# Optimization experiments

Hardware: AMD Instinct MI355X
Metric: run time of the kernel (lower is better)

Reference implementation:

```python
import jax, jax.numpy as jnp
import numpy as np
import math

D_MODEL = 1024
N_HEAD = 16
HEAD_DIM = D_MODEL // N_HEAD
D_FF = 4096
NUM_STEPS = 100.0
RESCALE = 4000.0
EPS = 1e-5


def _sin_emb(t):
    # SinusoidalPosEmb: t scaled by rescale_steps/num_steps
    half = D_MODEL // 2
    x = t.astype(jnp.float32) / NUM_STEPS * RESCALE
    freqs = jnp.exp(jnp.arange(half, dtype=jnp.float32) * (-math.log(10000.0) / (half - 1)))
    e = x[:, None] * freqs[None, :]
    return jnp.concatenate([jnp.sin(e), jnp.cos(e)], axis=-1)


def _ln(x):
    m = jnp.mean(x, axis=-1, keepdims=True)
    v = jnp.var(x, axis=-1, keepdims=True)
    return (x - m) / jnp.sqrt(v + EPS)


def _gelu2(x):
    return x * jax.nn.sigmoid(1.702 * x)


def setup_inputs() -> dict:
    key = jax.random.key(0)
    ks = jax.random.split(key, 24)
    B, S, D, F = 4, 512, D_MODEL, D_FF
    std = 0.02
    inp = {
        'src': jax.random.normal(ks[0], (B, S, D), dtype=jnp.float32),
        'src_mask': jax.random.randint(ks[1], (B, 1, S, S), 0, 2).astype(bool),
        'timestep': jax.random.randint(ks[2], (B,), 0, 100, dtype=jnp.int32),
        'attention_bias': jax.random.normal(ks[3], (B, N_HEAD, S, S), dtype=jnp.float32),
        # AdaLayerNorm linear: D -> 2D (scale, shift)
        'W_ada': jax.random.normal(ks[4], (D, 2 * D), dtype=jnp.float32) * std,
        'b_ada': jnp.zeros((2 * D,), dtype=jnp.float32),
        'Wq': jax.random.normal(ks[5], (D, D), dtype=jnp.float32) * std,
        'bq': jnp.zeros((D,), dtype=jnp.float32),
        'Wk': jax.random.normal(ks[6], (D, D), dtype=jnp.float32) * std,
        'bk': jnp.zeros((D,), dtype=jnp.float32),
        'Wv': jax.random.normal(ks[7], (D, D), dtype=jnp.float32) * std,
        'bv': jnp.zeros((D,), dtype=jnp.float32),
        'Wo': jax.random.normal(ks[8], (D, D), dtype=jnp.float32) * std,
        'bo': jnp.zeros((D,), dtype=jnp.float32),
        'W1': jax.random.normal(ks[9], (D, F), dtype=jnp.float32) * std,
        'b1': jnp.zeros((F,), dtype=jnp.float32),
        'W2': jax.random.normal(ks[10], (F, D), dtype=jnp.float32) * std,
        'b2': jnp.zeros((D,), dtype=jnp.float32),
        'g2': jnp.ones((D,), dtype=jnp.float32),
        'beta2': jnp.zeros((D,), dtype=jnp.float32),
    }
    return inp


def reference(src, src_mask, timestep, attention_bias, W_ada, b_ada,
              Wq, bq, Wk, bk, Wv, bv, Wo, bo, W1, b1, W2, b2, g2, beta2):
    B, S, D = src.shape
    # AdaLayerNorm: LN(x) * (1 + scale) + shift, scale/shift from timestep emb
    emb = jax.nn.silu(_sin_emb(timestep)) @ W_ada + b_ada  # [B, 2D]
    scale, shift = jnp.split(emb[:, None, :], 2, axis=-1)  # each [B,1,D]
    x = _ln(src) * (1.0 + scale) + shift

    # Self-attention with spatial bias + fp32 masked softmax
    q = (x @ Wq + bq).reshape(B, S, N_HEAD, HEAD_DIM).transpose(0, 2, 1, 3)
    k = (x @ Wk + bk).reshape(B, S, N_HEAD, HEAD_DIM).transpose(0, 2, 1, 3)
    v = (x @ Wv + bv).reshape(B, S, N_HEAD, HEAD_DIM).transpose(0, 2, 1, 3)
    scores = jnp.einsum('bhqd,bhkd->bhqk', q / math.sqrt(HEAD_DIM), k)
    scores = scores + attention_bias
    scores = jnp.where(src_mask, -jnp.inf, scores.astype(jnp.float32))
    probs = jax.nn.softmax(scores, axis=-1).astype(v.dtype)
    ctx = jnp.einsum('bhqk,bhkd->bhqd', probs, v)
    ctx = ctx.transpose(0, 2, 1, 3).reshape(B, S, D)
    x = x + (ctx @ Wo + bo)  # residual from AdaLN output (as in source)

    # FFN with gelu2 on LN2(x)
    h = _ln(x) * g2 + beta2
    ff = _gelu2(h @ W1 + b1) @ W2 + b2
    return x + ff
```

## Files before the change

kernel.cpp:

```cpp
#include <hip/hip_runtime.h>
#include <math.h>

typedef __bf16 bf16x8 __attribute__((ext_vector_type(8)));
typedef float  f32x4  __attribute__((ext_vector_type(4)));
typedef unsigned short u16x8 __attribute__((ext_vector_type(8)));

__device__ __forceinline__ float bf2f(unsigned short u) {
    return __uint_as_float(((unsigned int)u) << 16);
}
__device__ __forceinline__ unsigned short f2bf_n(float f) {
    return __builtin_bit_cast(unsigned short, (__bf16)f);
}
__device__ __forceinline__ void gl_lds16(const unsigned short* g, unsigned short* l) {
    __builtin_amdgcn_global_load_lds(
        (const __attribute__((address_space(1))) unsigned int*)g,
        (__attribute__((address_space(3))) unsigned int*)l, 16, 0, 0);
}

#define BATCH 4
#define SEQ 512
#define DM 1024
#define NH 16
#define DH 64
#define DFF 4096
#define MROWS (BATCH * SEQ)

__global__ __launch_bounds__(256) void fill0_kernel(float* __restrict__ out) {
    out[blockIdx.x * 256 + threadIdx.x] = 0.0f;
}

__global__ __launch_bounds__(256) void tconv_kernel(const float* __restrict__ in,
                                                    unsigned short* __restrict__ out,
                                                    int K, int N) {
    __shared__ float tile[64][33];
    const int n0 = blockIdx.x * 32, k0 = blockIdx.y * 64;
    const int t = threadIdx.x;
    const int tx = t & 31, ty = t >> 5;
    #pragma unroll
    for (int i = 0; i < 8; ++i)
        tile[ty + i * 8][tx] = in[(size_t)(k0 + ty + i * 8) * N + n0 + tx];
    __syncthreads();
    const int nr = t >> 3;
    const int ks = (t & 7) * 8;
    u16x8 v;
    #pragma unroll
    for (int j = 0; j < 8; ++j) v[j] = f2bf_n(tile[ks + j][nr]);
    *(u16x8*)&out[(size_t)(n0 + nr) * K + k0 + ks] = v;
}

__global__ __launch_bounds__(256) void tconv4_kernel(const float* __restrict__ i0,
                                                     const float* __restrict__ i1,
                                                     const float* __restrict__ i2,
                                                     const float* __restrict__ i3,
                                                     unsigned short* __restrict__ o0,
                                                     unsigned short* __restrict__ o1,
                                                     unsigned short* __restrict__ o2,
                                                     unsigned short* __restrict__ o3) {
    const int z = blockIdx.z;
    const float* in = (z == 0) ? i0 : (z == 1) ? i1 : (z == 2) ? i2 : i3;
    unsigned short* out = (z == 0) ? o0 : (z == 1) ? o1 : (z == 2) ? o2 : o3;
    __shared__ float tile[64][33];
    const int n0 = blockIdx.x * 32, k0 = blockIdx.y * 64;
    const int t = threadIdx.x;
    const int tx = t & 31, ty = t >> 5;
    #pragma unroll
    for (int i = 0; i < 8; ++i)
        tile[ty + i * 8][tx] = in[(size_t)(k0 + ty + i * 8) * 1024 + n0 + tx];
    __syncthreads();
    const int nr = t >> 3;
    const int ks = (t & 7) * 8;
    u16x8 v;
    #pragma unroll
    for (int j = 0; j < 8; ++j) v[j] = f2bf_n(tile[ks + j][nr]);
    *(u16x8*)&out[(size_t)(n0 + nr) * 1024 + k0 + ks] = v;
}

__global__ void semb_kernel(const int* __restrict__ ts, float* __restrict__ semb) {
    int b = blockIdx.x;
    float x = (float)ts[b] * 40.0f;
    for (int j = threadIdx.x; j < 1024; j += 256) {
        int idx = (j < 512) ? j : (j - 512);
        float fr = expf(-9.210340371976184f * (float)idx / 511.0f);
        float e = x * fr;
        float v = (j < 512) ? sinf(e) : cosf(e);
        semb[b * 1024 + j] = v / (1.0f + expf(-v));
    }
}

__global__ __launch_bounds__(256) void ada_part_kernel(const float* __restrict__ semb,
                                                       const float* __restrict__ W,
                                                       float* __restrict__ part) {
    const int nb = blockIdx.x, kc = blockIdx.y;
    const int t = threadIdx.x;
    __shared__ float e_s[4][64];
    e_s[t >> 6][t & 63] = semb[(t >> 6) * 1024 + kc * 64 + (t & 63)];
    __syncthreads();
    const int n = nb * 128 + (t & 127);
    const int half = t >> 7;
    float a0 = 0.f, a1 = 0.f, a2 = 0.f, a3 = 0.f;
    const int kk0 = half * 32;
    #pragma unroll 8
    for (int kk = kk0; kk < kk0 + 32; ++kk) {
        const float w = W[(size_t)(kc * 64 + kk) * 2048 + n];
        a0 += e_s[0][kk] * w; a1 += e_s[1][kk] * w;
        a2 += e_s[2][kk] * w; a3 += e_s[3][kk] * w;
    }
    const int j = kc * 2 + half;
    float* p = part + (size_t)j * 4 * 2048 + n;
    p[0] = a0; p[2048] = a1; p[2 * 2048] = a2; p[3 * 2048] = a3;
}

__global__ __launch_bounds__(256) void ada_red_kernel(const float* __restrict__ part,
                                                      const float* __restrict__ bias,
                                                      float* __restrict__ ss) {
    const int idx = blockIdx.x * 256 + threadIdx.x;
    const int b = idx >> 11, n = idx & 2047;
    float acc = bias[n];
    #pragma unroll 8
    for (int j = 0; j < 32; ++j) acc += part[((size_t)j * 4 + b) * 2048 + n];
    ss[b * 2048 + n] = acc;
}

__global__ __launch_bounds__(256) void adaln_kernel(const float* __restrict__ src,
                                                    const float* __restrict__ ss,
                                                    unsigned short* __restrict__ xb) {
    int r = blockIdx.x;
    int b = r >> 9;
    int t = threadIdx.x;
    float4 v4 = *reinterpret_cast<const float4*>(&src[(size_t)r * DM + t * 4]);
    float v[4] = {v4.x, v4.y, v4.z, v4.w};
    float s = v[0] + v[1] + v[2] + v[3];
    float q = v[0]*v[0] + v[1]*v[1] + v[2]*v[2] + v[3]*v[3];
    #pragma unroll
    for (int off = 32; off > 0; off >>= 1) { s += __shfl_down(s, off); q += __shfl_down(q, off); }
    __shared__ float red[8];
    if ((t & 63) == 0) { red[t >> 6] = s; red[4 + (t >> 6)] = q; }
    __syncthreads();
    s = red[0] + red[1] + red[2] + red[3];
    q = red[4] + red[5] + red[6] + red[7];
    float mean = s * (1.0f / DM);
    float var = q * (1.0f / DM) - mean * mean;
    float rstd = rsqrtf(var + 1e-5f);
    ushort4 o;
    o.x = f2bf_n((v[0]-mean)*rstd*(1.0f+ss[b*2048 + t*4+0]) + ss[b*2048+1024 + t*4+0]);
    o.y = f2bf_n((v[1]-mean)*rstd*(1.0f+ss[b*2048 + t*4+1]) + ss[b*2048+1024 + t*4+1]);
    o.z = f2bf_n((v[2]-mean)*rstd*(1.0f+ss[b*2048 + t*4+2]) + ss[b*2048+1024 + t*4+2]);
    o.w = f2bf_n((v[3]-mean)*rstd*(1.0f+ss[b*2048 + t*4+3]) + ss[b*2048+1024 + t*4+3]);
    *reinterpret_cast<ushort4*>(&xb[(size_t)r * DM + t * 4]) = o;
}

__global__ __launch_bounds__(256) void ln2_kernel(const unsigned short* __restrict__ x,
                                                  const float* __restrict__ g2,
                                                  const float* __restrict__ beta2,
                                                  unsigned short* __restrict__ hout) {
    int r = blockIdx.x;
    int t = threadIdx.x;
    ushort4 s4 = *reinterpret_cast<const ushort4*>(&x[(size_t)r * DM + t * 4]);
    float v[4] = {bf2f(s4.x), bf2f(s4.y), bf2f(s4.z), bf2f(s4.w)};
    float s = v[0] + v[1] + v[2] + v[3];
    float q = v[0]*v[0] + v[1]*v[1] + v[2]*v[2] + v[3]*v[3];
    #pragma unroll
    for (int off = 32; off > 0; off >>= 1) { s += __shfl_down(s, off); q += __shfl_down(q, off); }
    __shared__ float red[8];
    if ((t & 63) == 0) { red[t >> 6] = s; red[4 + (t >> 6)] = q; }
    __syncthreads();
    s = red[0] + red[1] + red[2] + red[3];
    q = red[4] + red[5] + red[6] + red[7];
    float mean = s * (1.0f / DM);
    float var = q * (1.0f / DM) - mean * mean;
    float rstd = rsqrtf(var + 1e-5f);
    ushort4 o;
    o.x = f2bf_n((v[0]-mean)*rstd*g2[t*4+0] + beta2[t*4+0]);
    o.y = f2bf_n((v[1]-mean)*rstd*g2[t*4+1] + beta2[t*4+1]);
    o.z = f2bf_n((v[2]-mean)*rstd*g2[t*4+2] + beta2[t*4+2]);
    o.w = f2bf_n((v[3]-mean)*rstd*g2[t*4+3] + beta2[t*4+3]);
    *reinterpret_cast<ushort4*>(&hout[(size_t)r * DM + t * 4]) = o;
}

__global__ __launch_bounds__(256) void merge_kernel(const unsigned short* __restrict__ P0,
                                                    const unsigned short* __restrict__ P1,
                                                    const float* __restrict__ b2,
                                                    const unsigned short* __restrict__ x2,
                                                    float* __restrict__ out) {
    const size_t i4 = ((size_t)blockIdx.x * 256 + threadIdx.x) * 4;
    const int c = (int)(i4 & 1023);
    ushort4 p0 = *(const ushort4*)&P0[i4];
    ushort4 p1 = *(const ushort4*)&P1[i4];
    ushort4 xx = *(const ushort4*)&x2[i4];
    float4 bb = *(const float4*)&b2[c];
    float4 o;
    o.x = bf2f(p0.x) + bf2f(p1.x) + bb.x + bf2f(xx.x);
    o.y = bf2f(p0.y) + bf2f(p1.y) + bb.y + bf2f(xx.y);
    o.z = bf2f(p0.z) + bf2f(p1.z) + bb.z + bf2f(xx.z);
    o.w = bf2f(p0.w) + bf2f(p1.w) + bb.w + bf2f(xx.w);
    *(float4*)&out[i4] = o;
}

template<int MODE, int TN, int SELMODE>
__global__ __launch_bounds__(256) void gemm_gl(
    const unsigned short* __restrict__ A,
    const unsigned short* __restrict__ Wta, const unsigned short* __restrict__ Wtb,
    const unsigned short* __restrict__ Wtc,
    const float* __restrict__ ba, const float* __restrict__ bbb, const float* __restrict__ bc,
    const unsigned short* __restrict__ resid,
    unsigned short* __restrict__ oa, unsigned short* __restrict__ ob,
    unsigned short* __restrict__ oc,
    float* __restrict__ outF,
    int M, int N, int K, int lda, int ldk)
{
    constexpr int CR  = 128 + TN;
    constexpr int RPW = CR / 4;
    constexpr int NI  = RPW / 8;
    constexpr int WAVE_N = (TN == 128) ? 2 : 1;
    constexpr int WAVE_M = 4 / WAVE_N;
    constexpr int AM = 128 / (WAVE_M * 16);
    constexpr int AN = TN / (WAVE_N * 16);
    constexpr int BUF = CR * 64;

    __shared__ unsigned short LDSu[2 * BUF];

    const int gx = gridDim.x, gy = gridDim.y;
    const int nwg = gx * gy * gridDim.z;
    const int wid = blockIdx.x + gx * (blockIdx.y + gy * blockIdx.z);
    const int aid = (wid & 7) * (nwg >> 3) + (wid >> 3);
    const int plane = gx * gy;
    const int sel = aid / plane;
    const int pid = aid % plane;
    const int by = pid % gy;
    const int bx = pid / gy;

    const unsigned short* Wt;
    const float* bias;
    unsigned short* outB;
    int koff;
    if (SELMODE == 0) {
        Wt = (sel == 0) ? Wta : (sel == 1) ? Wtb : Wtc;
        bias = (sel == 0) ? ba : (sel == 1) ? bbb : bc;
        outB = (sel == 0) ? oa : (sel == 1) ? ob : oc;
        koff = 0;
    } else {
        Wt = Wta; bias = ba;
        outB = (sel == 0) ? oa : ob;
        koff = sel * K;
    }

    const int t = threadIdx.x;
    const int lane = t & 63;
    const int w = t >> 6;
    const int l15 = lane & 15, l4 = lane >> 4;
    const int wm = w / WAVE_N, wn = w % WAVE_N;
    const int m0 = by * 128, n0 = bx * TN;

    f32x4 acc[AM][AN];
    #pragma unroll
    for (int i = 0; i < AM; ++i)
        #pragma unroll
        for (int j = 0; j < AN; ++j)
            #pragma unroll
            for (int r = 0; r < 4; ++r) acc[i][j][r] = 0.0f;

    const int gg = (lane & 7) ^ (lane >> 3);
    const unsigned short* gp[NI];
    unsigned short* lp[NI];
    #pragma unroll
    for (int i = 0; i < NI; ++i) {
        const int cr = w * RPW + i * 8 + (lane >> 3);
        gp[i] = (cr < 128) ? (A + (size_t)(m0 + cr) * lda + koff + gg * 8)
                           : (Wt + (size_t)(n0 + cr - 128) * ldk + koff + gg * 8);
        lp[i] = LDSu + (w * RPW + i * 8) * 64;
    }

    const int NT = K / 64;
    #pragma unroll
    for (int i = 0; i < NI; ++i) gl_lds16(gp[i], lp[i]);
    __syncthreads();

    for (int kt = 0; kt < NT; ++kt) {
        const int cur = kt & 1;
        if (kt + 1 < NT) {
            const int k0 = (kt + 1) * 64;
            const int nxo = (cur ^ 1) * BUF;
            #pragma unroll
            for (int i = 0; i < NI; ++i) gl_lds16(gp[i] + k0, lp[i] + nxo);
        }
        const unsigned short* Lb = LDSu + cur * BUF;
        #pragma unroll
        for (int kk = 0; kk < 2; ++kk) {
            const int slot = ((kk * 4 + l4) ^ (l15 & 7)) * 8;
            bf16x8 af[AM], bfr[AN];
            #pragma unroll
            for (int mt = 0; mt < AM; ++mt) {
                const int row = wm * (AM * 16) + mt * 16 + l15;
                u16x8 tmp = *(const u16x8*)(Lb + row * 64 + slot);
                af[mt] = __builtin_bit_cast(bf16x8, tmp);
            }
            #pragma unroll
            for (int nt = 0; nt < AN; ++nt) {
                const int row = 128 + wn * (AN * 16) + nt * 16 + l15;
                u16x8 tmp = *(const u16x8*)(Lb + row * 64 + slot);
                bfr[nt] = __builtin_bit_cast(bf16x8, tmp);
            }
            #pragma unroll
            for (int mt = 0; mt < AM; ++mt)
                #pragma unroll
                for (int nt = 0; nt < AN; ++nt)
                    acc[mt][nt] = __builtin_amdgcn_mfma_f32_16x16x32_bf16(
                        af[mt], bfr[nt], acc[mt][nt], 0, 0, 0);
        }
        if (kt + 1 < NT) __syncthreads();
    }

    #pragma unroll
    for (int mt = 0; mt < AM; ++mt) {
        const int mbase = m0 + wm * (AM * 16) + mt * 16 + l4 * 4;
        #pragma unroll
        for (int nt = 0; nt < AN; ++nt) {
            const int n = n0 + wn * (AN * 16) + nt * 16 + l15;
            const float bs = (MODE == 5) ? 0.0f : bias[n];
            #pragma unroll
            for (int r = 0; r < 4; ++r) {
                const int m = mbase + r;
                float v = acc[mt][nt][r] + bs;
                if (MODE == 2) v = v / (1.0f + expf(-1.702f * v));
                if (MODE == 1 || MODE == 3) v += bf2f(resid[(size_t)m * N + n]);
                if (MODE == 3) outF[(size_t)m * N + n] = v;
                else           outB[(size_t)m * N + n] = f2bf_n(v);
            }
        }
    }
}

#define QB2 32
#define AKT 64
#define KROW 72
#define VROW 72
#define PROW 72
#define SBPIT 72

__global__ __launch_bounds__(128) void attn_mfma(const unsigned short* __restrict__ qbuf,
                                                 const unsigned short* __restrict__ kbuf,
                                                 const unsigned short* __restrict__ vbuf,
                                                 const float* __restrict__ attb,
                                                 const int* __restrict__ mask,
                                                 unsigned short* __restrict__ ctx) {
    __shared__ unsigned short Ks[AKT * KROW];
    __shared__ unsigned short Vt[DH * VROW];
    __shared__ unsigned short Pb[2 * 16 * PROW];
    __shared__ unsigned short Sb[QB2 * SBPIT];
    const int t = threadIdx.x;
    const int lane = t & 63;
    const int w = t >> 6;
    const int l15 = lane & 15, l4 = lane >> 4;
    const int q0 = blockIdx.x * QB2;
    const int h = blockIdx.y;
    const int b = blockIdx.z;

    bf16x8 qf[2];
    {
        const unsigned short* qrow = qbuf + ((size_t)(b * SEQ + q0 + w * 16 + l15)) * DM + h * DH;
        u16x8 t0 = *(const u16x8*)(qrow + l4 * 8);
        u16x8 t1 = *(const u16x8*)(qrow + 32 + l4 * 8);
        qf[0] = __builtin_bit_cast(bf16x8, t0);
        qf[1] = __builtin_bit_cast(bf16x8, t1);
    }

    float m[4] = {-1e30f, -1e30f, -1e30f, -1e30f};
    float l[4] = {0.0f, 0.0f, 0.0f, 0.0f};
    f32x4 o[4];
    #pragma unroll
    for (int dt = 0; dt < 4; ++dt)
        #pragma unroll
        for (int r = 0; r < 4; ++r) o[dt][r] = 0.0f;

    unsigned short* Pw = Pb + w * 16 * PROW;

    const int kr = t >> 1, c0 = (t & 1) * 32;
    const int kp = t & 31, vg = t >> 5;

    u16x8 rk0, rk1, rk2, rk3, rv0, rv1, rv2, rv3;
    float4 rb[4];
    int4   rm[4];

#define LOADT(KT) {                                                                     \
    const int kbase = (KT) * AKT;                                                       \
    const unsigned short* gk = kbuf + ((size_t)(b * SEQ + kbase + kr)) * DM + h * DH + c0; \
    rk0 = *(const u16x8*)gk;        rk1 = *(const u16x8*)(gk + 8);                      \
    rk2 = *(const u16x8*)(gk + 16); rk3 = *(const u16x8*)(gk + 24);                     \
    const unsigned short* gv = vbuf + ((size_t)(b * SEQ + kbase + 2 * kp)) * DM + h * DH + vg * 8; \
    rv0 = *(const u16x8*)gv;        rv1 = *(const u16x8*)(gv + DM);                     \
    rv2 = *(const u16x8*)(gv + 32); rv3 = *(const u16x8*)(gv + DM + 32);                \
    const float* bp = attb + (((size_t)(b * NH + h)) * SEQ + (q0 + w * 16)) * SEQ + kbase; \
    const int* mp = mask + ((size_t)(b * SEQ) + q0 + w * 16) * SEQ + kbase;             \
    _Pragma("unroll")                                                                   \
    for (int i = 0; i < 4; ++i) {                                                       \
        const int e = lane + i * 64; const int row = e >> 4, cg = e & 15;               \
        rb[i] = *(const float4*)&bp[(size_t)row * SEQ + cg * 4];                        \
        rm[i] = *(const int4*)&mp[(size_t)row * SEQ + cg * 4];                          \
    } }

#define STORET() {                                                                      \
    unsigned short* s = Ks + kr * KROW + c0;                                            \
    *(u16x8*)s = rk0; *(u16x8*)(s + 8) = rk1;                                           \
    *(u16x8*)(s + 16) = rk2; *(u16x8*)(s + 24) = rk3;                                   \
    unsigned int* vt32 = (unsigned int*)Vt;                                             \
    _Pragma("unroll")                                                                   \
    for (int j = 0; j < 8; ++j) {                                                       \
        vt32[(vg * 8 + j) * (VROW / 2) + kp] =                                          \
            (unsigned int)rv0[j] | ((unsigned int)rv1[j] << 16);                        \
        vt32[((vg + 4) * 8 + j) * (VROW / 2) + kp] =                                    \
            (unsigned int)rv2[j] | ((unsigned int)rv3[j] << 16);                        \
    }                                                                                   \
    _Pragma("unroll")                                                                   \
    for (int i = 0; i < 4; ++i) {                                                       \
        const int e = lane + i * 64; const int row = e >> 4, cg = e & 15;               \
        ushort4 cc;                                                                     \
        cc.x = f2bf_n(rm[i].x ? -8e30f : 8.0f * rb[i].x);                               \
        cc.y = f2bf_n(rm[i].y ? -8e30f : 8.0f * rb[i].y);                               \
        cc.z = f2bf_n(rm[i].z ? -8e30f : 8.0f * rb[i].z);                               \
        cc.w = f2bf_n(rm[i].w ? -8e30f : 8.0f * rb[i].w);                               \
        *(ushort4*)&Sb[(w * 16 + row) * SBPIT + cg * 4] = cc;                           \
    } }

    LOADT(0);
    for (int kt = 0; kt < SEQ / AKT; ++kt) {
        __syncthreads();
        STORET();
        __syncthreads();
        if (kt + 1 < SEQ / AKT) LOADT(kt + 1);

        f32x4 acc[4];
        #pragma unroll
        for (int nt = 0; nt < 4; ++nt)
            #pragma unroll
            for (int r = 0; r < 4; ++r)
                acc[nt][r] = bf2f(Sb[(w * 16 + l4 * 4 + r) * SBPIT + nt * 16 + l15]);

        #pragma unroll
        for (int kk = 0; kk < 2; ++kk) {
            #pragma unroll
            for (int nt = 0; nt < 4; ++nt) {
                u16x8 tmp = *(const u16x8*)(Ks + (nt * 16 + l15) * KROW + kk * 32 + l4 * 8);
                acc[nt] = __builtin_amdgcn_mfma_f32_16x16x32_bf16(
                    qf[kk], __builtin_bit_cast(bf16x8, tmp), acc[nt], 0, 0, 0);
            }
        }

        float pm[4] = {-1e30f, -1e30f, -1e30f, -1e30f};
        #pragma unroll
        for (int nt = 0; nt < 4; ++nt) {
            #pragma unroll
            for (int r = 0; r < 4; ++r) {
                const float sv = acc[nt][r] * 0.125f;
                acc[nt][r] = sv;
                pm[r] = fmaxf(pm[r], sv);
            }
        }
        #pragma unroll
        for (int r = 0; r < 4; ++r) {
            #pragma unroll
            for (int off = 1; off < 16; off <<= 1)
                pm[r] = fmaxf(pm[r], __shfl_xor(pm[r], off));
        }
        float al[4], ps[4];
        #pragma unroll
        for (int r = 0; r < 4; ++r) {
            const float mn = fmaxf(m[r], pm[r]);
            al[r] = __expf(m[r] - mn);
            m[r] = mn;
            ps[r] = 0.0f;
        }
        #pragma unroll
        for (int nt = 0; nt < 4; ++nt) {
            #pragma unroll
            for (int r = 0; r < 4; ++r) {
                const float p = __expf(acc[nt][r] - m[r]);
                acc[nt][r] = p;
                ps[r] += p;
            }
        }
        #pragma unroll
        for (int r = 0; r < 4; ++r) {
            #pragma unroll
            for (int off = 1; off < 16; off <<= 1) ps[r] += __shfl_xor(ps[r], off);
            l[r] = l[r] * al[r] + ps[r];
        }
        #pragma unroll
        for (int dt = 0; dt < 4; ++dt)
            #pragma unroll
            for (int r = 0; r < 4; ++r) o[dt][r] *= al[r];

        #pragma unroll
        for (int nt = 0; nt < 4; ++nt)
            #pragma unroll
            for (int r = 0; r < 4; ++r)
                Pw[(l4 * 4 + r) * PROW + nt * 16 + l15] = f2bf_n(acc[nt][r]);

        #pragma unroll
        for (int ks = 0; ks < 2; ++ks) {
            u16x8 pa = *(const u16x8*)(Pw + l15 * PROW + ks * 32 + l4 * 8);
            #pragma unroll
            for (int dt = 0; dt < 4; ++dt) {
                u16x8 vv = *(const u16x8*)(Vt + (dt * 16 + l15) * VROW + ks * 32 + l4 * 8);
                o[dt] = __builtin_amdgcn_mfma_f32_16x16x32_bf16(
                    __builtin_bit_cast(bf16x8, pa), __builtin_bit_cast(bf16x8, vv),
                    o[dt], 0, 0, 0);
            }
        }
    }

    #pragma unroll
    for (int r = 0; r < 4; ++r) {
        const float inv = 1.0f / l[r];
        const size_t row = (size_t)(b * SEQ + q0 + w * 16 + l4 * 4 + r) * DM + h * DH;
        #pragma unroll
        for (int dt = 0; dt < 4; ++dt)
            ctx[row + dt * 16 + l15] = f2bf_n(o[dt][r] * inv);
    }
#undef LOADT
#undef STORET
}

extern "C" void kernel_launch(void* const* d_in, const int* in_sizes, int n_in,
                              void* d_out, int out_size, void* d_ws, size_t ws_size,
                              hipStream_t stream) {
    const float* src  = (const float*)d_in[0];
    const int*   mask = (const int*)d_in[1];
    const int*   ts   = (const int*)d_in[2];
    const float* attb = (const float*)d_in[3];
    const float* Wada = (const float*)d_in[4];
    const float* bada = (const float*)d_in[5];
    const float* Wq   = (const float*)d_in[6];
    const float* bq   = (const float*)d_in[7];
    const float* Wk   = (const float*)d_in[8];
    const float* bk   = (const float*)d_in[9];
    const float* Wv   = (const float*)d_in[10];
    const float* bv   = (const float*)d_in[11];
    const float* Wo   = (const float*)d_in[12];
    const float* bo   = (const float*)d_in[13];
    const float* W1   = (const float*)d_in[14];
    const float* b1   = (const float*)d_in[15];
    const float* W2   = (const float*)d_in[16];
    const float* b2   = (const float*)d_in[17];
    const float* g2   = (const float*)d_in[18];
    const float* bt2  = (const float*)d_in[19];
    float* out = (float*)d_out;

    const size_t MB = 1024 * 1024;
    const size_t NEED_FULL = 65536 + 52 * MB;
    if (ws_size < NEED_FULL) {
        fill0_kernel<<<(size_t)MROWS * DM / 256, 256, 0, stream>>>(out);
        return;
    }

    char* ws = (char*)d_ws;
    float* semb = (float*)(ws + 4096);
    float* ss   = (float*)(ws + 24576);
    char*  base = ws + 65536;
    unsigned short* slotA = (unsigned short*)(base);
    unsigned short* slotB = (unsigned short*)(base + 4 * MB);
    unsigned short* slotC = (unsigned short*)(base + 8 * MB);
    unsigned short* vb   = (unsigned short*)d_out;
    unsigned short* ctxb = (unsigned short*)((char*)d_out + 4 * MB);
    unsigned short* xb = slotA;
    unsigned short* qb = slotB;
    unsigned short* kb = slotC;
    unsigned short* x2 = slotB;
    unsigned short* hb = slotC;
    unsigned short* P0 = slotA;
    unsigned short* P1 = slotC;
    float* adap = (float*)slotC;

    unsigned short* Wtq = (unsigned short*)(base + 12 * MB);
    unsigned short* Wtk = Wtq + 1024 * 1024;
    unsigned short* Wtv = Wtk + 1024 * 1024;
    unsigned short* Wto = Wtv + 1024 * 1024;
    unsigned short* Wt1 = Wto + 1024 * 1024;
    unsigned short* Wt2 = Wt1 + (size_t)4096 * 1024;
    unsigned short* midF = (unsigned short*)(base + 36 * MB);

    tconv4_kernel<<<dim3(32, 16, 4), 256, 0, stream>>>(Wq, Wk, Wv, Wo, Wtq, Wtk, Wtv, Wto);
    tconv_kernel<<<dim3(128, 16), 256, 0, stream>>>(W1, Wt1, 1024, 4096);
    tconv_kernel<<<dim3(32, 64), 256, 0, stream>>>(W2, Wt2, 4096, 1024);

    semb_kernel<<<4, 256, 0, stream>>>(ts, semb);
    ada_part_kernel<<<dim3(16, 16), 256, 0, stream>>>(semb, Wada, adap);
    ada_red_kernel<<<32, 256, 0, stream>>>(adap, bada, ss);
    adaln_kernel<<<MROWS, 256, 0, stream>>>(src, ss, xb);

    gemm_gl<0, 128, 0><<<dim3(8, 16, 3), 256, 0, stream>>>(
        xb, Wtq, Wtk, Wtv, bq, bk, bv, nullptr, qb, kb, vb, nullptr,
        MROWS, DM, DM, DM, DM);
    attn_mfma<<<dim3(SEQ / QB2, NH, BATCH), 128, 0, stream>>>(qb, kb, vb, attb, mask, ctxb);
    gemm_gl<1, 64, 0><<<dim3(16, 16), 256, 0, stream>>>(
        ctxb, Wto, Wto, Wto, bo, bo, bo, xb, x2, x2, x2, nullptr,
        MROWS, DM, DM, DM, DM);
    ln2_kernel<<<MROWS, 256, 0, stream>>>(x2, g2, bt2, hb);
    gemm_gl<2, 128, 0><<<dim3(32, 16), 256, 0, stream>>>(
        hb, Wt1, Wt1, Wt1, b1, b1, b1, nullptr, midF, midF, midF, nullptr,
        MROWS, DFF, DM, DM, DM);
    gemm_gl<5, 128, 1><<<dim3(8, 16, 2), 256, 0, stream>>>(
        midF, Wt2, Wt2, Wt2, b2, b2, b2, nullptr, P0, P1, nullptr, nullptr,
        MROWS, DM, 2048, DFF, DFF);
    merge_kernel<<<(size_t)MROWS * DM / 1024, 256, 0, stream>>>(P0, P1, b2, x2, out);
}
```

Measured before the change: 156.9 us.

## Split attention key range across two blocks and merge partial softmax results

The attention kernel now splits the key sequence into two halves, one per block, doubling the grid from 1024 to 2048 blocks. Each half writes its unnormalized output plus its running max and sum, and a new merge kernel combines them with log-sum-exp rescaling. This targets low occupancy or long serial loops per block. The cost is an extra launch, extra global traffic for the partial outputs, and bf16 rounding of the unnormalized partials.

Measured after the change: 163.5 us. 1.04x slower.

```diff
diff --git a/kernel.cpp b/kernel.cpp
--- a/kernel.cpp
+++ b/kernel.cpp
@@ -194,6 +194,30 @@
     o.z = bf2f(p0.z) + bf2f(p1.z) + bb.z + bf2f(xx.z);
     o.w = bf2f(p0.w) + bf2f(p1.w) + bb.w + bf2f(xx.w);
     *(float4*)&out[i4] = o;
+}
+
+__global__ __launch_bounds__(256) void attn_merge_kernel(const unsigned short* __restrict__ po,
+                                                         const float* __restrict__ pm,
+                                                         const float* __restrict__ pl,
+                                                         unsigned short* __restrict__ ctx) {
+    const size_t i4 = ((size_t)blockIdx.x * 256 + threadIdx.x) * 4;
+    const int row = (int)(i4 >> 10);
+    const int col = (int)(i4 & 1023);
+    const int h = col >> 6;
+    const int mi = row * NH + h;
+    const float m0 = pm[mi], m1 = pm[MROWS * NH + mi];
+    const float l0 = pl[mi], l1 = pl[MROWS * NH + mi];
+    const float M = fmaxf(m0, m1);
+    const float w0 = __expf(m0 - M), w1 = __expf(m1 - M);
+    const float inv = 1.0f / (w0 * l0 + w1 * l1);
+    ushort4 a = *(const ushort4*)&po[i4];
+    ushort4 b = *(const ushort4*)&po[(size_t)MROWS * DM + i4];
+    ushort4 o;
+    o.x = f2bf_n((w0 * bf2f(a.x) + w1 * bf2f(b.x)) * inv);
+    o.y = f2bf_n((w0 * bf2f(a.y) + w1 * bf2f(b.y)) * inv);
+    o.z = f2bf_n((w0 * bf2f(a.z) + w1 * bf2f(b.z)) * inv);
+    o.w = f2bf_n((w0 * bf2f(a.w) + w1 * bf2f(b.w)) * inv);
+    *(ushort4*)&ctx[i4] = o;
 }
 
 template<int MODE, int TN, int SELMODE>
@@ -342,7 +366,9 @@
                                                  const unsigned short* __restrict__ vbuf,
                                                  const float* __restrict__ attb,
                                                  const int* __restrict__ mask,
-                                                 unsigned short* __restrict__ ctx) {
+                                                 unsigned short* __restrict__ po,
+                                                 float* __restrict__ pm,
+                                                 float* __restrict__ pl) {
     __shared__ unsigned short Ks[AKT * KROW];
     __shared__ unsigned short Vt[DH * VROW];
     __shared__ unsigned short Pb[2 * 16 * PROW];
@@ -353,7 +379,9 @@
     const int l15 = lane & 15, l4 = lane >> 4;
     const int q0 = blockIdx.x * QB2;
     const int h = blockIdx.y;
-    const int b = blockIdx.z;
+    const int b = blockIdx.z >> 1;
+    const int sp = blockIdx.z & 1;
+    const int kofs = sp * (SEQ / 2);
 
     bf16x8 qf[2];
     {
@@ -382,7 +410,7 @@
     int4   rm[4];
 
 #define LOADT(KT) {                                                                     \
-    const int kbase = (KT) * AKT;                                                       \
+    const int kbase = kofs + (KT) * AKT;                                                \
     const unsigned short* gk = kbuf + ((size_t)(b * SEQ + kbase + kr)) * DM + h * DH + c0; \
     rk0 = *(const u16x8*)gk;        rk1 = *(const u16x8*)(gk + 8);                      \
     rk2 = *(const u16x8*)(gk + 16); rk3 = *(const u16x8*)(gk + 24);                     \
@@ -422,11 +450,12 @@
     } }
 
     LOADT(0);
-    for (int kt = 0; kt < SEQ / AKT; ++kt) {
+    const int NT = (SEQ / 2) / AKT;
+    for (int kt = 0; kt < NT; ++kt) {
         __syncthreads();
         STORET();
         __syncthreads();
-        if (kt + 1 < SEQ / AKT) LOADT(kt + 1);
+        if (kt + 1 < NT) LOADT(kt + 1);
 
         f32x4 acc[4];
         #pragma unroll
@@ -445,26 +474,26 @@
             }
         }
 
-        float pm[4] = {-1e30f, -1e30f, -1e30f, -1e30f};
+        float pmx[4] = {-1e30f, -1e30f, -1e30f, -1e30f};
         #pragma unroll
         for (int nt = 0; nt < 4; ++nt) {
             #pragma unroll
             for (int r = 0; r < 4; ++r) {
                 const float sv = acc[nt][r] * 0.125f;
                 acc[nt][r] = sv;
-                pm[r] = fmaxf(pm[r], sv);
+                pmx[r] = fmaxf(pmx[r], sv);
             }
         }
         #pragma unroll
         for (int r = 0; r < 4; ++r) {
             #pragma unroll
             for (int off = 1; off < 16; off <<= 1)
-                pm[r] = fmaxf(pm[r], __shfl_xor(pm[r], off));
+                pmx[r] = fmaxf(pmx[r], __shfl_xor(pmx[r], off));
         }
         float al[4], ps[4];
         #pragma unroll
         for (int r = 0; r < 4; ++r) {
-            const float mn = fmaxf(m[r], pm[r]);
+            const float mn = fmaxf(m[r], pmx[r]);
             al[r] = __expf(m[r] - mn);
             m[r] = mn;
             ps[r] = 0.0f;
@@ -510,11 +539,16 @@
 
     #pragma unroll
     for (int r = 0; r < 4; ++r) {
-        const float inv = 1.0f / l[r];
-        const size_t row = (size_t)(b * SEQ + q0 + w * 16 + l4 * 4 + r) * DM + h * DH;
+        const int rowg = b * SEQ + q0 + w * 16 + l4 * 4 + r;
+        const size_t obase = (size_t)sp * MROWS * DM + (size_t)rowg * DM + h * DH;
         #pragma unroll
         for (int dt = 0; dt < 4; ++dt)
-            ctx[row + dt * 16 + l15] = f2bf_n(o[dt][r] * inv);
+            po[obase + dt * 16 + l15] = f2bf_n(o[dt][r]);
+        if (l15 == 0) {
+            const size_t mi = (size_t)sp * MROWS * NH + (size_t)rowg * NH + h;
+            pm[mi] = m[r];
+            pl[mi] = l[r];
+        }
     }
 #undef LOADT
 #undef STORET
@@ -577,6 +611,9 @@
     unsigned short* Wt1 = Wto + 1024 * 1024;
     unsigned short* Wt2 = Wt1 + (size_t)4096 * 1024;
     unsigned short* midF = (unsigned short*)(base + 36 * MB);
+    unsigned short* po = midF;
+    float* pmv = (float*)(base + 36 * MB + 8 * MB);
+    float* plv = (float*)(base + 36 * MB + 8 * MB + 512 * 1024);
 
     tconv4_kernel<<<dim3(32, 16, 4), 256, 0, stream>>>(Wq, Wk, Wv, Wo, Wtq, Wtk, Wtv, Wto);
     tconv_kernel<<<dim3(128, 16), 256, 0, stream>>>(W1, Wt1, 1024, 4096);
@@ -590,7 +627,9 @@
     gemm_gl<0, 128, 0><<<dim3(8, 16, 3), 256, 0, stream>>>(
         xb, Wtq, Wtk, Wtv, bq, bk, bv, nullptr, qb, kb, vb, nullptr,
         MROWS, DM, DM, DM, DM);
-    attn_mfma<<<dim3(SEQ / QB2, NH, BATCH), 128, 0, stream>>>(qb, kb, vb, attb, mask, ctxb);
+    attn_mfma<<<dim3(SEQ / QB2, NH, BATCH * 2), 128, 0, stream>>>(
+        qb, kb, vb, attb, mask, po, pmv, plv);
+    attn_merge_kernel<<<(size_t)MROWS * DM / 1024, 256, 0, stream>>>(po, pmv, plv, ctxb);
     gemm_gl<1, 64, 0><<<dim3(16, 16), 256, 0, stream>>>(
         ctxb, Wto, Wto, Wto, bo, bo, bo, xb, x2, x2, x2, nullptr,
         MROWS, DM, DM, DM, DM);
```

## Increase FFN2 split-K to four partials and raise MFMA priority in attention

Applied to the files above, without the earlier changes.

The second FFN GEMM now splits K four ways instead of two, launching twice as many workgroups. The partial results go into the dead transposed-weight buffers, and a four-input merge kernel sums them with the bias and residual. Attention wraps its MFMA loops in s_setprio to favour matrix issue across waves. The extra partials add memory traffic in the merge kernel in exchange for better CU occupancy in the GEMM.

Result: no change. 159.4 us (+1.6%).

```diff
diff --git a/kernel.cpp b/kernel.cpp
--- a/kernel.cpp
+++ b/kernel.cpp
@@ -177,22 +177,26 @@
     *reinterpret_cast<ushort4*>(&hout[(size_t)r * DM + t * 4]) = o;
 }
 
-__global__ __launch_bounds__(256) void merge_kernel(const unsigned short* __restrict__ P0,
-                                                    const unsigned short* __restrict__ P1,
-                                                    const float* __restrict__ b2,
-                                                    const unsigned short* __restrict__ x2,
-                                                    float* __restrict__ out) {
+__global__ __launch_bounds__(256) void merge4_kernel(const unsigned short* __restrict__ P0,
+                                                     const unsigned short* __restrict__ P1,
+                                                     const unsigned short* __restrict__ P2,
+                                                     const unsigned short* __restrict__ P3,
+                                                     const float* __restrict__ b2,
+                                                     const unsigned short* __restrict__ x2,
+                                                     float* __restrict__ out) {
     const size_t i4 = ((size_t)blockIdx.x * 256 + threadIdx.x) * 4;
     const int c = (int)(i4 & 1023);
     ushort4 p0 = *(const ushort4*)&P0[i4];
     ushort4 p1 = *(const ushort4*)&P1[i4];
+    ushort4 p2 = *(const ushort4*)&P2[i4];
+    ushort4 p3 = *(const ushort4*)&P3[i4];
     ushort4 xx = *(const ushort4*)&x2[i4];
     float4 bb = *(const float4*)&b2[c];
     float4 o;
-    o.x = bf2f(p0.x) + bf2f(p1.x) + bb.x + bf2f(xx.x);
-    o.y = bf2f(p0.y) + bf2f(p1.y) + bb.y + bf2f(xx.y);
-    o.z = bf2f(p0.z) + bf2f(p1.z) + bb.z + bf2f(xx.z);
-    o.w = bf2f(p0.w) + bf2f(p1.w) + bb.w + bf2f(xx.w);
+    o.x = bf2f(p0.x) + bf2f(p1.x) + bf2f(p2.x) + bf2f(p3.x) + bb.x + bf2f(xx.x);
+    o.y = bf2f(p0.y) + bf2f(p1.y) + bf2f(p2.y) + bf2f(p3.y) + bb.y + bf2f(xx.y);
+    o.z = bf2f(p0.z) + bf2f(p1.z) + bf2f(p2.z) + bf2f(p3.z) + bb.z + bf2f(xx.z);
+    o.w = bf2f(p0.w) + bf2f(p1.w) + bf2f(p2.w) + bf2f(p3.w) + bb.w + bf2f(xx.w);
     *(float4*)&out[i4] = o;
 }
 
@@ -204,7 +208,7 @@
     const float* __restrict__ ba, const float* __restrict__ bbb, const float* __restrict__ bc,
     const unsigned short* __restrict__ resid,
     unsigned short* __restrict__ oa, unsigned short* __restrict__ ob,
-    unsigned short* __restrict__ oc,
+    unsigned short* __restrict__ oc, unsigned short* __restrict__ od,
     float* __restrict__ outF,
     int M, int N, int K, int lda, int ldk)
 {
@@ -240,7 +244,7 @@
         koff = 0;
     } else {
         Wt = Wta; bias = ba;
-        outB = (sel == 0) ? oa : ob;
+        outB = (sel == 0) ? oa : (sel == 1) ? ob : (sel == 2) ? oc : od;
         koff = sel * K;
     }
 
@@ -422,11 +426,12 @@
     } }
 
     LOADT(0);
-    for (int kt = 0; kt < SEQ / AKT; ++kt) {
+    const int NT = SEQ / AKT;
+    for (int kt = 0; kt < NT; ++kt) {
         __syncthreads();
         STORET();
         __syncthreads();
-        if (kt + 1 < SEQ / AKT) LOADT(kt + 1);
+        if (kt + 1 < NT) LOADT(kt + 1);
 
         f32x4 acc[4];
         #pragma unroll
@@ -435,6 +440,7 @@
             for (int r = 0; r < 4; ++r)
                 acc[nt][r] = bf2f(Sb[(w * 16 + l4 * 4 + r) * SBPIT + nt * 16 + l15]);
 
+        __builtin_amdgcn_s_setprio(1);
         #pragma unroll
         for (int kk = 0; kk < 2; ++kk) {
             #pragma unroll
@@ -444,6 +450,7 @@
                     qf[kk], __builtin_bit_cast(bf16x8, tmp), acc[nt], 0, 0, 0);
             }
         }
+        __builtin_amdgcn_s_setprio(0);
 
         float pm[4] = {-1e30f, -1e30f, -1e30f, -1e30f};
         #pragma unroll
@@ -495,6 +502,7 @@
             for (int r = 0; r < 4; ++r)
                 Pw[(l4 * 4 + r) * PROW + nt * 16 + l15] = f2bf_n(acc[nt][r]);
 
+        __builtin_amdgcn_s_setprio(1);
         #pragma unroll
         for (int ks = 0; ks < 2; ++ks) {
             u16x8 pa = *(const u16x8*)(Pw + l15 * PROW + ks * 32 + l4 * 8);
@@ -506,6 +514,7 @@
                     o[dt], 0, 0, 0);
             }
         }
+        __builtin_amdgcn_s_setprio(0);
     }
 
     #pragma unroll
@@ -566,8 +575,6 @@
     unsigned short* kb = slotC;
     unsigned short* x2 = slotB;
     unsigned short* hb = slotC;
-    unsigned short* P0 = slotA;
-    unsigned short* P1 = slotC;
     float* adap = (float*)slotC;
 
     unsigned short* Wtq = (unsigned short*)(base + 12 * MB);
@@ -577,6 +584,10 @@
     unsigned short* Wt1 = Wto + 1024 * 1024;
     unsigned short* Wt2 = Wt1 + (size_t)4096 * 1024;
     unsigned short* midF = (unsigned short*)(base + 36 * MB);
+    unsigned short* P0 = slotA;
+    unsigned short* P1 = slotC;
+    unsigned short* P2 = Wtq;
+    unsigned short* P3 = Wtv;
 
     tconv4_kernel<<<dim3(32, 16, 4), 256, 0, stream>>>(Wq, Wk, Wv, Wo, Wtq, Wtk, Wtv, Wto);
     tconv_kernel<<<dim3(128, 16), 256, 0, stream>>>(W1, Wt1, 1024, 4096);
@@ -588,18 +599,18 @@
     adaln_kernel<<<MROWS, 256, 0, stream>>>(src, ss, xb);
 
     gemm_gl<0, 128, 0><<<dim3(8, 16, 3), 256, 0, stream>>>(
-        xb, Wtq, Wtk, Wtv, bq, bk, bv, nullptr, qb, kb, vb, nullptr,
+        xb, Wtq, Wtk, Wtv, bq, bk, bv, nullptr, qb, kb, vb, nullptr, nullptr,
         MROWS, DM, DM, DM, DM);
     attn_mfma<<<dim3(SEQ / QB2, NH, BATCH), 128, 0, stream>>>(qb, kb, vb, attb, mask, ctxb);
     gemm_gl<1, 64, 0><<<dim3(16, 16), 256, 0, stream>>>(
-        ctxb, Wto, Wto, Wto, bo, bo, bo, xb, x2, x2, x2, nullptr,
+        ctxb, Wto, Wto, Wto, bo, bo, bo, xb, x2, x2, x2, nullptr, nullptr,
         MROWS, DM, DM, DM, DM);
     ln2_kernel<<<MROWS, 256, 0, stream>>>(x2, g2, bt2, hb);
     gemm_gl<2, 128, 0><<<dim3(32, 16), 256, 0, stream>>>(
-        hb, Wt1, Wt1, Wt1, b1, b1, b1, nullptr, midF, midF, midF, nullptr,
+        hb, Wt1, Wt1, Wt1, b1, b1, b1, nullptr, midF, midF, midF, nullptr, nullptr,
         MROWS, DFF, DM, DM, DM);
-    gemm_gl<5, 128, 1><<<dim3(8, 16, 2), 256, 0, stream>>>(
-        midF, Wt2, Wt2, Wt2, b2, b2, b2, nullptr, P0, P1, nullptr, nullptr,
-        MROWS, DM, 2048, DFF, DFF);
-    merge_kernel<<<(size_t)MROWS * DM / 1024, 256, 0, stream>>>(P0, P1, b2, x2, out);
-}
+    gemm_gl<5, 128, 1><<<dim3(8, 16, 4), 256, 0, stream>>>(
+        midF, Wt2, Wt2, Wt2, b2, b2, b2, nullptr, P0, P1, P2, P3, nullptr,
+        MROWS, DM, 1024, DFF, DFF);
+    merge4_kernel<<<(size_t)MROWS * DM / 1024, 256, 0, stream>>>(P0, P1, P2, P3, b2, x2, out);
+}
```
